# Kernel optimization log

Hardware: AMD Instinct MI355X
Metric: run time of the kernel (lower is better)

Reference implementation:

```python
import jax, jax.numpy as jnp
import numpy as np

N, T, c = 8192, 121, 40
C, P = 384, 12

def setup_inputs() -> dict:
    key = jax.random.key(0)
    k1, k2, k3 = jax.random.split(key, 3)
    waveforms = jax.random.normal(k1, (N, T, c), dtype=jnp.float32)
    max_channels = jax.random.randint(k2, (N,), 0, C, dtype=jnp.int64)
    # values in [0, c]; value == c indexes the inf pad column (no parent)
    parents_index = jax.random.randint(k3, (C, c, P), 0, c + 1, dtype=jnp.int64)
    return {"waveforms": waveforms, "max_channels": max_channels, "parents_index": parents_index}

def reference(waveforms, max_channels, parents_index):
    n = waveforms.shape[0]
    # peak-to-peak per channel: [N, c]
    ptps = waveforms.max(axis=1) - waveforms.min(axis=1)
    # pad with +inf sentinel column so missing parents never bind the min
    pad_ptps = jnp.pad(ptps, ((0, 0), (0, 1)), constant_values=jnp.inf)  # [N, c+1]
    pidx = parents_index[max_channels]                                   # [N, c, P]
    parent_ptps = pad_ptps[jnp.arange(n)[:, None, None], pidx]           # [N, c, P]
    parent_min_ptps = parent_ptps.min(axis=2)                            # [N, c]
    rescaling = jnp.minimum(parent_min_ptps / ptps, 1.0)                 # [N, c]
    decreasing_ptps = ptps * rescaling
    decreasing_waveforms = waveforms * rescaling[:, None, :]
    return decreasing_waveforms, decreasing_ptps
```

## Files before the change

### kernel.cpp

```cpp
#include <hip/hip_runtime.h>
#include <math.h>


#define N_T 121
#define N_C 40
#define N_P 12
#define TPB 256
#define WF_ELEMS (N_T * N_C)
#define WF_QUADS (WF_ELEMS / 4)
#define FULL_K   (WF_QUADS / TPB)
#define TAIL_Q   (WF_QUADS - FULL_K * TPB)

typedef float f32x4 __attribute__((ext_vector_type(4)));

#define GLOAD_LDS16(g, l)                                              \
    __builtin_amdgcn_global_load_lds(                                  \
        (const __attribute__((address_space(1))) void*)(g),            \
        (__attribute__((address_space(3))) void*)(l), 16, 0, 0)

__global__ __launch_bounds__(TPB) void enforce_decrease_kernel(
    const float* __restrict__ waveforms,
    const int*   __restrict__ max_channels,
    const int*   __restrict__ parents_index,
    float*       __restrict__ out,
    int n_total)
{
    __shared__ float wf[WF_ELEMS];
    __shared__ float pmx[6 * N_C];
    __shared__ float pmn[6 * N_C];
    __shared__ float ptp[N_C];
    __shared__ float resc[N_C];

    const int n   = blockIdx.x;
    const int tid = threadIdx.x;

    const float* src = waveforms + (size_t)n * WF_ELEMS;
    #pragma unroll
    for (int k = 0; k < FULL_K; ++k) {
        const int q = tid + TPB * k;
        GLOAD_LDS16(src + 4 * q, wf + 4 * q);
    }
    if (tid < TAIL_Q) {
        const int q = FULL_K * TPB + tid;
        GLOAD_LDS16(src + 4 * q, wf + 4 * q);
    }
    __syncthreads();

    if (tid < 6 * N_C) {
        const int ch = tid % N_C;
        const int g  = tid / N_C;
        float mx = -INFINITY, mn = INFINITY;
        for (int t = g; t < N_T; t += 6) {
            const float v = wf[t * N_C + ch];
            mx = fmaxf(mx, v);
            mn = fminf(mn, v);
        }
        pmx[tid] = mx;
        pmn[tid] = mn;
    }
    __syncthreads();

    if (tid < N_C) {
        float mx = pmx[tid], mn = pmn[tid];
        #pragma unroll
        for (int g = 1; g < 6; ++g) {
            mx = fmaxf(mx, pmx[g * N_C + tid]);
            mn = fminf(mn, pmn[g * N_C + tid]);
        }
        ptp[tid] = mx - mn;
    }
    __syncthreads();

    if (tid < N_C) {
        const int  mc   = max_channels[n];
        const int* prow = parents_index + mc * (N_C * N_P) + tid * N_P;
        float minp = INFINITY;
        #pragma unroll
        for (int p = 0; p < N_P; ++p) {
            const int idx = prow[p];
            minp = fminf(minp, (idx >= N_C) ? INFINITY : ptp[idx]);
        }
        const float r = fminf(minp / ptp[tid], 1.0f);
        resc[tid] = r;
        __builtin_nontemporal_store(
            ptp[tid] * r,
            out + (size_t)n_total * WF_ELEMS + (size_t)n * N_C + tid);
    }
    __syncthreads();

    const f32x4* wf4  = (const f32x4*)wf;
    f32x4*       dst4 = (f32x4*)(out + (size_t)n * WF_ELEMS);
    #pragma unroll
    for (int i = tid; i < WF_QUADS; i += TPB) {
        f32x4 v = wf4[i];
        const int ch0 = (i * 4) % N_C;
        v.x *= resc[ch0];
        v.y *= resc[ch0 + 1];
        v.z *= resc[ch0 + 2];
        v.w *= resc[ch0 + 3];
        __builtin_nontemporal_store(v, &dst4[i]);
    }
}

extern "C" void kernel_launch(void* const* d_in, const int* in_sizes, int n_in,
                              void* d_out, int out_size, void* d_ws, size_t ws_size,
                              hipStream_t stream) {
    const float* waveforms     = (const float*)d_in[0];
    const int*   max_channels  = (const int*)d_in[1];
    const int*   parents_index = (const int*)d_in[2];
    float*       out           = (float*)d_out;

    const int n = in_sizes[1];

    enforce_decrease_kernel<<<dim3(n), dim3(TPB), 0, stream>>>(
        waveforms, max_channels, parents_index, out, n);
}
```

Before: 55.87 us.

## Persistent blocks with double-buffered LDS prefetch of next waveform

Switches from one block per waveform to 1024 persistent blocks, each handling 8 waveforms with a two-slot LDS buffer. The next waveform's global-to-LDS load is issued before the current one's reduction and scaling, so loading overlaps compute. Some __syncthreads are replaced by barriers that wait only on LDS counters, and the reduction split drops from 6 to 4 groups. LDS per block doubles (about 39KB), which limits resident blocks per CU. The grid is hardcoded to N/8, so it silently assumes n equals NBLK*SPB.

Result: slower. 58.24 us (+4.2%).

```diff
diff --git a/kernel.cpp b/kernel.cpp
--- a/kernel.cpp
+++ b/kernel.cpp
@@ -10,6 +10,8 @@
 #define WF_QUADS (WF_ELEMS / 4)
 #define FULL_K   (WF_QUADS / TPB)
 #define TAIL_Q   (WF_QUADS - FULL_K * TPB)
+#define NBLK 1024
+#define SPB  8
 
 typedef float f32x4 __attribute__((ext_vector_type(4)));
 
@@ -18,87 +20,116 @@
         (const __attribute__((address_space(1))) void*)(g),            \
         (__attribute__((address_space(3))) void*)(l), 16, 0, 0)
 
-__global__ __launch_bounds__(TPB) void enforce_decrease_kernel(
+#define BAR_LGKM() do {                                                \
+    asm volatile("s_waitcnt lgkmcnt(0)" ::: "memory");                 \
+    __builtin_amdgcn_s_barrier();                                      \
+} while (0)
+
+__device__ __forceinline__ void stage(const float* __restrict__ src,
+                                      float* dst, int tid) {
+    #pragma unroll
+    for (int k = 0; k < FULL_K; ++k) {
+        const int q = tid + TPB * k;
+        GLOAD_LDS16(src + 4 * q, dst + 4 * q);
+    }
+    if (tid < TAIL_Q) {
+        const int q = FULL_K * TPB + tid;
+        GLOAD_LDS16(src + 4 * q, dst + 4 * q);
+    }
+}
+
+__global__ __launch_bounds__(TPB, 4) void enforce_decrease_kernel(
     const float* __restrict__ waveforms,
     const int*   __restrict__ max_channels,
     const int*   __restrict__ parents_index,
     float*       __restrict__ out,
     int n_total)
 {
-    __shared__ float wf[WF_ELEMS];
-    __shared__ float pmx[6 * N_C];
-    __shared__ float pmn[6 * N_C];
+    __shared__ float wf[2][WF_ELEMS];
+    __shared__ float pmx[4 * N_C];
+    __shared__ float pmn[4 * N_C];
     __shared__ float ptp[N_C];
     __shared__ float resc[N_C];
 
-    const int n   = blockIdx.x;
     const int tid = threadIdx.x;
+    const int bid = blockIdx.x;
 
-    const float* src = waveforms + (size_t)n * WF_ELEMS;
-    #pragma unroll
-    for (int k = 0; k < FULL_K; ++k) {
-        const int q = tid + TPB * k;
-        GLOAD_LDS16(src + 4 * q, wf + 4 * q);
-    }
-    if (tid < TAIL_Q) {
-        const int q = FULL_K * TPB + tid;
-        GLOAD_LDS16(src + 4 * q, wf + 4 * q);
-    }
-    __syncthreads();
+    stage(waveforms + (size_t)bid * WF_ELEMS, wf[0], tid);
 
-    if (tid < 6 * N_C) {
-        const int ch = tid % N_C;
-        const int g  = tid / N_C;
-        float mx = -INFINITY, mn = INFINITY;
-        for (int t = g; t < N_T; t += 6) {
-            const float v = wf[t * N_C + ch];
-            mx = fmaxf(mx, v);
-            mn = fminf(mn, v);
+    for (int g = 0; g < SPB; ++g) {
+        const int    n    = bid + g * NBLK;
+        float*       wcur = wf[g & 1];
+
+        __syncthreads();
+
+        if (g + 1 < SPB)
+            stage(waveforms + (size_t)(n + NBLK) * WF_ELEMS, wf[(g + 1) & 1], tid);
+
+        if (tid < 4 * N_C) {
+            const int ch = tid % N_C;
+            const int g4 = tid / N_C;
+            float mx = -INFINITY, mn = INFINITY;
+            for (int t = g4; t < N_T; t += 4) {
+                const float v = wcur[t * N_C + ch];
+                mx = fmaxf(mx, v);
+                mn = fminf(mn, v);
+            }
+            pmx[tid] = mx;
+            pmn[tid] = mn;
         }
-        pmx[tid] = mx;
-        pmn[tid] = mn;
-    }
-    __syncthreads();
+        BAR_LGKM();
 
-    if (tid < N_C) {
-        float mx = pmx[tid], mn = pmn[tid];
+        if (tid < N_C) {
+            float mx = pmx[tid], mn = pmn[tid];
+            #pragma unroll
+            for (int q = 1; q < 4; ++q) {
+                mx = fmaxf(mx, pmx[q * N_C + tid]);
+                mn = fminf(mn, pmn[q * N_C + tid]);
+            }
+            ptp[tid] = mx - mn;
+        }
+        BAR_LGKM();
+
+        if (tid < N_C) {
+            const int  mc   = max_channels[n];
+            const int* prow = parents_index + mc * (N_C * N_P) + tid * N_P;
+            float minp = INFINITY;
+            #pragma unroll
+            for (int p = 0; p < N_P; ++p) {
+                const int idx = prow[p];
+                minp = fminf(minp, (idx >= N_C) ? INFINITY : ptp[idx]);
+            }
+            const float r = fminf(minp / ptp[tid], 1.0f);
+            resc[tid] = r;
+            __builtin_nontemporal_store(
+                ptp[tid] * r,
+                out + (size_t)n_total * WF_ELEMS + (size_t)n * N_C + tid);
+        }
+        BAR_LGKM();
+
+        const f32x4* w4   = (const f32x4*)wcur;
+        f32x4*       dst4 = (f32x4*)(out + (size_t)n * WF_ELEMS);
         #pragma unroll
-        for (int g = 1; g < 6; ++g) {
-            mx = fmaxf(mx, pmx[g * N_C + tid]);
-            mn = fminf(mn, pmn[g * N_C + tid]);
+        for (int k = 0; k < FULL_K; ++k) {
+            const int i = tid + TPB * k;
+            f32x4 v = w4[i];
+            const int ch0 = (i * 4) % N_C;
+            v.x *= resc[ch0];
+            v.y *= resc[ch0 + 1];
+            v.z *= resc[ch0 + 2];
+            v.w *= resc[ch0 + 3];
+            __builtin_nontemporal_store(v, &dst4[i]);
         }
-        ptp[tid] = mx - mn;
-    }
-    __syncthreads();
-
-    if (tid < N_C) {
-        const int  mc   = max_channels[n];
-        const int* prow = parents_index + mc * (N_C * N_P) + tid * N_P;
-        float minp = INFINITY;
-        #pragma unroll
-        for (int p = 0; p < N_P; ++p) {
-            const int idx = prow[p];
-            minp = fminf(minp, (idx >= N_C) ? INFINITY : ptp[idx]);
+        if (tid < TAIL_Q) {
+            const int i = FULL_K * TPB + tid;
+            f32x4 v = w4[i];
+            const int ch0 = (i * 4) % N_C;
+            v.x *= resc[ch0];
+            v.y *= resc[ch0 + 1];
+            v.z *= resc[ch0 + 2];
+            v.w *= resc[ch0 + 3];
+            __builtin_nontemporal_store(v, &dst4[i]);
         }
-        const float r = fminf(minp / ptp[tid], 1.0f);
-        resc[tid] = r;
-        __builtin_nontemporal_store(
-            ptp[tid] * r,
-            out + (size_t)n_total * WF_ELEMS + (size_t)n * N_C + tid);
-    }
-    __syncthreads();
-
-    const f32x4* wf4  = (const f32x4*)wf;
-    f32x4*       dst4 = (f32x4*)(out + (size_t)n * WF_ELEMS);
-    #pragma unroll
-    for (int i = tid; i < WF_QUADS; i += TPB) {
-        f32x4 v = wf4[i];
-        const int ch0 = (i * 4) % N_C;
-        v.x *= resc[ch0];
-        v.y *= resc[ch0 + 1];
-        v.z *= resc[ch0 + 2];
-        v.w *= resc[ch0 + 3];
-        __builtin_nontemporal_store(v, &dst4[i]);
     }
 }
 
@@ -112,6 +143,6 @@
 
     const int n = in_sizes[1];
 
-    enforce_decrease_kernel<<<dim3(n), dim3(TPB), 0, stream>>>(
+    enforce_decrease_kernel<<<dim3(NBLK), dim3(TPB), 0, stream>>>(
         waveforms, max_channels, parents_index, out, n);
 }
```

## Split fused kernel into ptp/rescale kernel and separate scaling kernel

Applied to the files above, without the earlier changes.

Splits the single kernel into two launches. The first computes per-channel peak-to-peak and the rescaling factors, writing the factors to a workspace buffer. The second re-reads the waveforms from global memory and applies the factors with vectorized loads and stores. This shortens each block's lifetime and LDS hold time, which may raise occupancy, but it reads the waveforms twice and adds a second launch.

New measurement: 81.67 us. 46.2% more time.

```diff
diff --git a/kernel.cpp b/kernel.cpp
--- a/kernel.cpp
+++ b/kernel.cpp
@@ -18,18 +18,18 @@
         (const __attribute__((address_space(1))) void*)(g),            \
         (__attribute__((address_space(3))) void*)(l), 16, 0, 0)
 
-__global__ __launch_bounds__(TPB) void enforce_decrease_kernel(
+__global__ __launch_bounds__(TPB) void ptps_kernel(
     const float* __restrict__ waveforms,
     const int*   __restrict__ max_channels,
     const int*   __restrict__ parents_index,
     float*       __restrict__ out,
+    float*       __restrict__ resc_ws,
     int n_total)
 {
     __shared__ float wf[WF_ELEMS];
     __shared__ float pmx[6 * N_C];
     __shared__ float pmn[6 * N_C];
     __shared__ float ptp[N_C];
-    __shared__ float resc[N_C];
 
     const int n   = blockIdx.x;
     const int tid = threadIdx.x;
@@ -81,24 +81,42 @@
             minp = fminf(minp, (idx >= N_C) ? INFINITY : ptp[idx]);
         }
         const float r = fminf(minp / ptp[tid], 1.0f);
-        resc[tid] = r;
+        resc_ws[(size_t)n * N_C + tid] = r;
         __builtin_nontemporal_store(
             ptp[tid] * r,
             out + (size_t)n_total * WF_ELEMS + (size_t)n * N_C + tid);
     }
-    __syncthreads();
+}
 
-    const f32x4* wf4  = (const f32x4*)wf;
-    f32x4*       dst4 = (f32x4*)(out + (size_t)n * WF_ELEMS);
+__global__ __launch_bounds__(TPB) void scale_kernel(
+    const float* __restrict__ waveforms,
+    const float* __restrict__ resc_ws,
+    float*       __restrict__ out)
+{
+    const int n   = blockIdx.x;
+    const int tid = threadIdx.x;
+
+    const f32x4* in4 = (const f32x4*)(waveforms + (size_t)n * WF_ELEMS);
+    f32x4*       o4  = (f32x4*)(out + (size_t)n * WF_ELEMS);
+    const f32x4* r4  = (const f32x4*)(resc_ws + (size_t)n * N_C);
+
+    int m = tid % 10;
     #pragma unroll
-    for (int i = tid; i < WF_QUADS; i += TPB) {
-        f32x4 v = wf4[i];
-        const int ch0 = (i * 4) % N_C;
-        v.x *= resc[ch0];
-        v.y *= resc[ch0 + 1];
-        v.z *= resc[ch0 + 2];
-        v.w *= resc[ch0 + 3];
-        __builtin_nontemporal_store(v, &dst4[i]);
+    for (int k = 0; k < FULL_K; ++k) {
+        const int i = tid + TPB * k;
+        const f32x4 s = r4[m];
+        f32x4 v = in4[i];
+        v.x *= s.x; v.y *= s.y; v.z *= s.z; v.w *= s.w;
+        __builtin_nontemporal_store(v, &o4[i]);
+        m += 6;
+        if (m >= 10) m -= 10;
+    }
+    if (tid < TAIL_Q) {
+        const int i = FULL_K * TPB + tid;
+        const f32x4 s = r4[m];
+        f32x4 v = in4[i];
+        v.x *= s.x; v.y *= s.y; v.z *= s.z; v.w *= s.w;
+        __builtin_nontemporal_store(v, &o4[i]);
     }
 }
 
@@ -109,9 +127,12 @@
     const int*   max_channels  = (const int*)d_in[1];
     const int*   parents_index = (const int*)d_in[2];
     float*       out           = (float*)d_out;
+    float*       resc_ws       = (float*)d_ws;
 
     const int n = in_sizes[1];
 
-    enforce_decrease_kernel<<<dim3(n), dim3(TPB), 0, stream>>>(
-        waveforms, max_channels, parents_index, out, n);
+    ptps_kernel<<<dim3(n), dim3(TPB), 0, stream>>>(
+        waveforms, max_channels, parents_index, out, resc_ws, n);
+    scale_kernel<<<dim3(n), dim3(TPB), 0, stream>>>(
+        waveforms, resc_ws, out);
 }
```
